# Optimization experiments

Measured on AMD Instinct MI355X. Metric: run time of the kernel, lower is better.

The kernel has to match this reference:

```python
import jax, jax.numpy as jnp
import numpy as np
from jax import lax

ALIVE_THRESHOLD = 0.1
GROWTH_BOOST = 1.0  # forward default arg

_SX = jnp.array([[-1., 0., 1.], [-2., 0., 2.], [-1., 0., 1.]], dtype=jnp.float32)
_SY = jnp.array([[-1., -2., -1.], [0., 0., 0.], [1., 2., 1.]], dtype=jnp.float32)


def _depthwise3x3(x, k):
    # x: [B,C,H,W], k: [3,3] -> depthwise conv, padding 1 (SAME)
    C = x.shape[1]
    w = jnp.tile(k[None, None], (C, 1, 1, 1))  # [C,1,3,3]
    return lax.conv_general_dilated(
        x, w, window_strides=(1, 1), padding='SAME',
        dimension_numbers=('NCHW', 'OIHW', 'NCHW'), feature_group_count=C)


def _avg_pool3x3(x):
    # torch avg_pool2d(k=3, stride=1, pad=1, count_include_pad=True) == sum window / 9 with zero pad
    w = jnp.ones((1, 1, 3, 3), dtype=x.dtype) / 9.0
    return lax.conv_general_dilated(
        x, w, window_strides=(1, 1), padding='SAME',
        dimension_numbers=('NCHW', 'OIHW', 'NCHW'))


def setup_inputs() -> dict:
    key = jax.random.key(0)
    ks = jax.random.split(key, 5)
    B, C, H, W = 16, 8, 512, 512
    x = jax.random.normal(ks[0], (B, C, H, W), dtype=jnp.float32)
    # kaiming_normal_(a=0.3) -> std = sqrt(2/(1+a^2)) / sqrt(fan_in)
    gain = float(np.sqrt(2.0 / (1.0 + 0.3 ** 2)))
    w1 = jax.random.normal(ks[1], (32, 24), dtype=jnp.float32) * (gain / np.sqrt(24))
    w2 = jax.random.normal(ks[2], (32, 32), dtype=jnp.float32) * (gain / np.sqrt(32))
    w3 = jax.random.normal(ks[3], (8, 32), dtype=jnp.float32) * (gain / np.sqrt(32))
    b1 = jnp.full((32,), 0.05, dtype=jnp.float32)
    b2 = jnp.full((32,), 0.05, dtype=jnp.float32)
    b3 = jnp.full((8,), 0.05, dtype=jnp.float32)
    growth_rate = jnp.array([0.3], dtype=jnp.float32)
    return {'x': x, 'w1': w1, 'b1': b1, 'w2': w2, 'b2': b2,
            'w3': w3, 'b3': b3, 'growth_rate': growth_rate}


def reference(x, w1, b1, w2, b2, w3, b3, growth_rate):
    # perceive: [x, sobel_x(x), sobel_y(x)] -> [B, 3C, H, W]
    perceived = jnp.concatenate([x, _depthwise3x3(x, _SX), _depthwise3x3(x, _SY)], axis=1)
    # per-pixel MLP (1x1 convs)
    h = jax.nn.relu(jnp.einsum('bchw,oc->bohw', perceived, w1) + b1[None, :, None, None])
    h = jax.nn.relu(jnp.einsum('bchw,oc->bohw', h, w2) + b2[None, :, None, None])
    dx = jnp.einsum('bchw,oc->bohw', h, w3) + b3[None, :, None, None]
    dx = dx * growth_rate[0] * GROWTH_BOOST
    # alive masking / growth zones
    alive_mask = (x[:, 3:4] > ALIVE_THRESHOLD).astype(x.dtype)
    alive_ratio = jnp.mean(alive_mask)
    neighbor_alive = _avg_pool3x3(alive_mask)
    growth_zones = (neighbor_alive > 0.01).astype(x.dtype) * 0.2  # [B,1,H,W]
    boost = jnp.where(alive_ratio < 0.2, growth_zones, jnp.zeros_like(growth_zones))
    dx = jnp.concatenate([dx[:, :3], dx[:, 3:4] + boost, dx[:, 4:]], axis=1)
    new_x = jnp.clip(x + dx, -1.0, 1.0)
    alpha = jnp.clip(new_x[:, 3:4], 0.0, 1.0)
    return jnp.concatenate([new_x[:, :3], alpha, new_x[:, 4:]], axis=1)
```

## Files before the change

kernel.cpp:

```cpp
#include <hip/hip_runtime.h>

namespace {

constexpr int kH = 512, kW = 512, kB = 16, kC = 8;
constexpr int kHW = kH * kW;
constexpr int kBS = kC * kHW;
constexpr int TW = 64, TH = 4;
constexpr int TWP = TW + 2, THP = TH + 2;

__global__ __launch_bounds__(256)
void alive_count_kernel(const float* __restrict__ x, int* __restrict__ cnt) {
    __shared__ int sdata[4];
    const int tid = threadIdx.x;
    const int total4 = kB * kHW / 4;
    int idx = blockIdx.x * 256 + tid;
    const int stride = gridDim.x * 256;
    int local = 0;
    const float4* x4 = (const float4*)x;
    for (int i = idx; i < total4; i += stride) {
        int b = i >> 16;
        int off = i & 65535;
        float4 v = x4[(size_t)b * (kBS / 4) + (3 * kHW / 4) + off];
        local += (v.x > 0.1f) + (v.y > 0.1f) + (v.z > 0.1f) + (v.w > 0.1f);
    }
    for (int off = 32; off > 0; off >>= 1)
        local += __shfl_down(local, off, 64);
    if ((tid & 63) == 0) sdata[tid >> 6] = local;
    __syncthreads();
    if (tid == 0) atomicAdd(cnt, sdata[0] + sdata[1] + sdata[2] + sdata[3]);
}

__global__ __launch_bounds__(256, 2)
void nca_fused_kernel(const float* __restrict__ x,
                      const float* __restrict__ w1, const float* __restrict__ b1,
                      const float* __restrict__ w2, const float* __restrict__ b2,
                      const float* __restrict__ w3, const float* __restrict__ b3,
                      const float* __restrict__ growth,
                      const int* __restrict__ alive_cnt,
                      float* __restrict__ out) {
    __shared__ float tile[kC][THP][TWP];

    const int w0 = blockIdx.x * TW;
    const int h0 = blockIdx.y * TH;
    const int b  = blockIdx.z;
    const int tid = threadIdx.x;
    const float* xb = x + b * kBS;

    constexpr int TILE_N = kC * THP * TWP;
    for (int i = tid; i < TILE_N; i += 256) {
        int c  = i / (THP * TWP);
        int r  = i - c * (THP * TWP);
        int hh = r / TWP;
        int ww = r - hh * TWP;
        int gh = h0 + hh - 1;
        int gw = w0 + ww - 1;
        float v = 0.0f;
        if ((unsigned)gh < (unsigned)kH && (unsigned)gw < (unsigned)kW)
            v = xb[c * kHW + gh * kW + gw];
        (&tile[0][0][0])[i] = v;
    }
    __syncthreads();

    const int ww = tid & (TW - 1);
    const int hh = tid >> 6;

    float p[24];
    int nalive = 0;
#pragma unroll
    for (int c = 0; c < kC; ++c) {
        float a00 = tile[c][hh    ][ww], a01 = tile[c][hh    ][ww + 1], a02 = tile[c][hh    ][ww + 2];
        float a10 = tile[c][hh + 1][ww], a11 = tile[c][hh + 1][ww + 1], a12 = tile[c][hh + 1][ww + 2];
        float a20 = tile[c][hh + 2][ww], a21 = tile[c][hh + 2][ww + 1], a22 = tile[c][hh + 2][ww + 2];
        p[c]      = a11;
        p[8 + c]  = (a02 - a00) + 2.0f * (a12 - a10) + (a22 - a20);
        p[16 + c] = (a20 - a00) + 2.0f * (a21 - a01) + (a22 - a02);
        if (c == 3) {
            nalive = (a00 > 0.1f) + (a01 > 0.1f) + (a02 > 0.1f)
                   + (a10 > 0.1f) + (a11 > 0.1f) + (a12 > 0.1f)
                   + (a20 > 0.1f) + (a21 > 0.1f) + (a22 > 0.1f);
        }
    }

    float h1[32];
#pragma unroll
    for (int o = 0; o < 32; ++o) {
        float acc = b1[o];
#pragma unroll
        for (int i2 = 0; i2 < 24; ++i2) acc = fmaf(w1[o * 24 + i2], p[i2], acc);
        h1[o] = fmaxf(acc, 0.0f);
    }
    float h2[32];
#pragma unroll
    for (int o = 0; o < 32; ++o) {
        float acc = b2[o];
#pragma unroll
        for (int i2 = 0; i2 < 32; ++i2) acc = fmaf(w2[o * 32 + i2], h1[i2], acc);
        h2[o] = fmaxf(acc, 0.0f);
    }
    float d[8];
#pragma unroll
    for (int o = 0; o < 8; ++o) {
        float acc = b3[o];
#pragma unroll
        for (int i2 = 0; i2 < 32; ++i2) acc = fmaf(w3[o * 32 + i2], h2[i2], acc);
        d[o] = acc;
    }

    const float g = growth[0];
    const float ratio = (float)(*alive_cnt) * (1.0f / 4194304.0f);
    const float boost = (ratio < 0.2f && nalive > 0) ? 0.2f : 0.0f;

    float* ob = out + b * kBS + (h0 + hh) * kW + (w0 + ww);
#pragma unroll
    for (int c = 0; c < kC; ++c) {
        float v = p[c] + d[c] * g + ((c == 3) ? boost : 0.0f);
        const float lo = (c == 3) ? 0.0f : -1.0f;
        v = fminf(fmaxf(v, lo), 1.0f);
        ob[c * kHW] = v;
    }
}

}

extern "C" void kernel_launch(void* const* d_in, const int* in_sizes, int n_in,
                              void* d_out, int out_size, void* d_ws, size_t ws_size,
                              hipStream_t stream) {
    const float* x  = (const float*)d_in[0];
    const float* w1 = (const float*)d_in[1];
    const float* b1 = (const float*)d_in[2];
    const float* w2 = (const float*)d_in[3];
    const float* b2 = (const float*)d_in[4];
    const float* w3 = (const float*)d_in[5];
    const float* b3 = (const float*)d_in[6];
    const float* gr = (const float*)d_in[7];
    float* out = (float*)d_out;
    int* cnt = (int*)d_ws;

    hipMemsetAsync(cnt, 0, sizeof(int), stream);
    alive_count_kernel<<<256, 256, 0, stream>>>(x, cnt);
    dim3 grid(kW / TW, kH / TH, kB);
    nca_fused_kernel<<<grid, 256, 0, stream>>>(x, w1, b1, w2, b2, w3, b3, gr, cnt, out);
}
```

Measured before the change: 479.8 us.

## Run per-pixel MLP on bf16 MFMA with split hi/lo precision emulation

Replaces the scalar FMA loops for the three per-pixel 1x1-conv layers with 16x16x32 bf16 MFMA instructions. Each fp32 operand is split into bf16 hi and lo parts, and four MFMAs per product approximate fp32 accuracy. Layer outputs are rearranged into B fragments with ds_bpermute, and weights are preloaded into register fragments. The alive-count kernel grid is also raised from 256 to 2048 blocks. This aims to cut the dominant VALU FMA cost, at the price of extra conversion, permute and LDS traffic and some loss of precision.

```diff
diff --git a/kernel.cpp b/kernel.cpp
--- a/kernel.cpp
+++ b/kernel.cpp
@@ -1,6 +1,10 @@
 #include <hip/hip_runtime.h>
 
 namespace {
+
+typedef __attribute__((ext_vector_type(8))) short short8;
+typedef __attribute__((ext_vector_type(4))) float f32x4;
+typedef __attribute__((ext_vector_type(4))) unsigned int uint4v;
 
 constexpr int kH = 512, kW = 512, kB = 16, kC = 8;
 constexpr int kHW = kH * kW;
@@ -30,7 +34,66 @@
     if (tid == 0) atomicAdd(cnt, sdata[0] + sdata[1] + sdata[2] + sdata[3]);
 }
 
-__global__ __launch_bounds__(256, 2)
+__device__ inline unsigned int cvt_pk_bf16(float a, float b) {
+    unsigned int r;
+    asm("v_cvt_pk_bf16_f32 %0, %1, %2" : "=v"(r) : "v"(a), "v"(b));
+    return r;
+}
+__device__ inline void split_pair(float a, float b, unsigned int& h, unsigned int& l) {
+    h = cvt_pk_bf16(a, b);
+    float ra = a - __builtin_bit_cast(float, h << 16);
+    float rb = b - __builtin_bit_cast(float, h & 0xffff0000u);
+    l = cvt_pk_bf16(ra, rb);
+}
+__device__ inline short8 frag_of(unsigned int u0, unsigned int u1,
+                                 unsigned int u2, unsigned int u3) {
+    uint4v u = {u0, u1, u2, u3};
+    return __builtin_bit_cast(short8, u);
+}
+__device__ inline void split_frag(f32x4 a, f32x4 b, short8& hi, short8& lo) {
+    unsigned int h0, h1, h2, h3, l0, l1, l2, l3;
+    split_pair(a.x, a.y, h0, l0);
+    split_pair(a.z, a.w, h1, l1);
+    split_pair(b.x, b.y, h2, l2);
+    split_pair(b.z, b.w, h3, l3);
+    hi = frag_of(h0, h1, h2, h3);
+    lo = frag_of(l0, l1, l2, l3);
+}
+__device__ inline f32x4 mfma4(short8 wh, short8 wl, short8 bh, short8 bl, f32x4 acc) {
+    acc = __builtin_amdgcn_mfma_f32_16x16x32_bf16(wh, bh, acc, 0, 0, 0);
+    acc = __builtin_amdgcn_mfma_f32_16x16x32_bf16(wh, bl, acc, 0, 0, 0);
+    acc = __builtin_amdgcn_mfma_f32_16x16x32_bf16(wl, bh, acc, 0, 0, 0);
+    acc = __builtin_amdgcn_mfma_f32_16x16x32_bf16(wl, bl, acc, 0, 0, 0);
+    return acc;
+}
+__device__ inline f32x4 relu4(f32x4 v) {
+    v.x = fmaxf(v.x, 0.f); v.y = fmaxf(v.y, 0.f);
+    v.z = fmaxf(v.z, 0.f); v.w = fmaxf(v.w, 0.f);
+    return v;
+}
+__device__ inline void transpose_to_bfrag(f32x4 v0, f32x4 v1, int i1, int i2,
+                                          bool oddq, bool lowq,
+                                          short8& bh, short8& bl) {
+    unsigned int Ah, Al, Bh, Bl, Ch, Cl, Dh, Dl;
+    split_pair(v0.x, v0.y, Ah, Al);
+    split_pair(v0.z, v0.w, Bh, Bl);
+    split_pair(v1.x, v1.y, Ch, Cl);
+    split_pair(v1.z, v1.w, Dh, Dl);
+    int f1h = __builtin_amdgcn_ds_bpermute(i1, (int)(oddq ? Ch : Ah));
+    int f2h = __builtin_amdgcn_ds_bpermute(i2, (int)(oddq ? Ah : Ch));
+    int f3h = __builtin_amdgcn_ds_bpermute(i1, (int)(oddq ? Dh : Bh));
+    int f4h = __builtin_amdgcn_ds_bpermute(i2, (int)(oddq ? Bh : Dh));
+    int f1l = __builtin_amdgcn_ds_bpermute(i1, (int)(oddq ? Cl : Al));
+    int f2l = __builtin_amdgcn_ds_bpermute(i2, (int)(oddq ? Al : Cl));
+    int f3l = __builtin_amdgcn_ds_bpermute(i1, (int)(oddq ? Dl : Bl));
+    int f4l = __builtin_amdgcn_ds_bpermute(i2, (int)(oddq ? Bl : Dl));
+    bh = frag_of(lowq ? (unsigned)f1h : (unsigned)f2h, lowq ? (unsigned)f3h : (unsigned)f4h,
+                 lowq ? (unsigned)f2h : (unsigned)f1h, lowq ? (unsigned)f4h : (unsigned)f3h);
+    bl = frag_of(lowq ? (unsigned)f1l : (unsigned)f2l, lowq ? (unsigned)f3l : (unsigned)f4l,
+                 lowq ? (unsigned)f2l : (unsigned)f1l, lowq ? (unsigned)f4l : (unsigned)f3l);
+}
+
+__global__ __launch_bounds__(256)
 void nca_fused_kernel(const float* __restrict__ x,
                       const float* __restrict__ w1, const float* __restrict__ b1,
                       const float* __restrict__ w2, const float* __restrict__ b2,
@@ -39,21 +102,60 @@
                       const int* __restrict__ alive_cnt,
                       float* __restrict__ out) {
     __shared__ float tile[kC][THP][TWP];
+    __shared__ __align__(16) unsigned int s_hi[4][64][20];
+    __shared__ __align__(16) unsigned int s_lo[4][64][20];
+    __shared__ __align__(16) float s_d[4][64][8];
 
     const int w0 = blockIdx.x * TW;
     const int h0 = blockIdx.y * TH;
     const int b  = blockIdx.z;
     const int tid = threadIdx.x;
+    const int lane = tid & 63;
+    const int wv = tid >> 6;
+    const int m = lane & 15;
+    const int q = lane >> 4;
+    const bool oddq = (q & 1) != 0;
+    const bool lowq = q < 2;
+    const int brq = ((q & 1) << 1) | (q >> 1);
+    const int i1 = (m + 16 * brq) << 2;
+    const int i2 = (m + 16 * (brq ^ 1)) << 2;
     const float* xb = x + b * kBS;
+
+    f32x4 zero4 = {0.f, 0.f, 0.f, 0.f};
+    short8 w1h[2], w1l[2], w2h[2], w2l[2], w3h, w3l;
+    f32x4 bias1[2], bias2[2], bias3;
+#pragma unroll
+    for (int mo = 0; mo < 2; ++mo) {
+        int o = mo * 16 + m;
+        int off = (q < 3) ? (o * 24 + q * 8) : 0;
+        f32x4 wa = *(const f32x4*)(w1 + off);
+        f32x4 wb = *(const f32x4*)(w1 + off + 4);
+        if (q == 3) { wa = zero4; wb = zero4; }
+        split_frag(wa, wb, w1h[mo], w1l[mo]);
+        f32x4 wc = *(const f32x4*)(w2 + o * 32 + q * 8);
+        f32x4 wd = *(const f32x4*)(w2 + o * 32 + q * 8 + 4);
+        split_frag(wc, wd, w2h[mo], w2l[mo]);
+        bias1[mo] = *(const f32x4*)(b1 + mo * 16 + q * 4);
+        bias2[mo] = *(const f32x4*)(b2 + mo * 16 + q * 4);
+    }
+    {
+        int off3 = (m < 8) ? (m * 32 + q * 8) : 0;
+        f32x4 wa = *(const f32x4*)(w3 + off3);
+        f32x4 wb = *(const f32x4*)(w3 + off3 + 4);
+        if (m >= 8) { wa = zero4; wb = zero4; }
+        split_frag(wa, wb, w3h, w3l);
+        bias3 = zero4;
+        if (lowq) bias3 = *(const f32x4*)(b3 + q * 4);
+    }
 
     constexpr int TILE_N = kC * THP * TWP;
     for (int i = tid; i < TILE_N; i += 256) {
         int c  = i / (THP * TWP);
-        int r  = i - c * (THP * TWP);
-        int hh = r / TWP;
-        int ww = r - hh * TWP;
-        int gh = h0 + hh - 1;
-        int gw = w0 + ww - 1;
+        int rr = i - c * (THP * TWP);
+        int th = rr / TWP;
+        int tw = rr - th * TWP;
+        int gh = h0 + th - 1;
+        int gw = w0 + tw - 1;
         float v = 0.0f;
         if ((unsigned)gh < (unsigned)kH && (unsigned)gw < (unsigned)kW)
             v = xb[c * kHW + gh * kW + gw];
@@ -61,14 +163,13 @@
     }
     __syncthreads();
 
-    const int ww = tid & (TW - 1);
-    const int hh = tid >> 6;
-
+    const int ww = lane;
+    const int hh = wv;
     float p[24];
     int nalive = 0;
 #pragma unroll
     for (int c = 0; c < kC; ++c) {
-        float a00 = tile[c][hh    ][ww], a01 = tile[c][hh    ][ww + 1], a02 = tile[c][hh    ][ww + 2];
+        float a00 = tile[c][hh][ww],     a01 = tile[c][hh][ww + 1],     a02 = tile[c][hh][ww + 2];
         float a10 = tile[c][hh + 1][ww], a11 = tile[c][hh + 1][ww + 1], a12 = tile[c][hh + 1][ww + 2];
         float a20 = tile[c][hh + 2][ww], a21 = tile[c][hh + 2][ww + 1], a22 = tile[c][hh + 2][ww + 2];
         p[c]      = a11;
@@ -80,40 +181,58 @@
                    + (a20 > 0.1f) + (a21 > 0.1f) + (a22 > 0.1f);
         }
     }
-
-    float h1[32];
-#pragma unroll
-    for (int o = 0; o < 32; ++o) {
-        float acc = b1[o];
-#pragma unroll
-        for (int i2 = 0; i2 < 24; ++i2) acc = fmaf(w1[o * 24 + i2], p[i2], acc);
-        h1[o] = fmaxf(acc, 0.0f);
-    }
-    float h2[32];
-#pragma unroll
-    for (int o = 0; o < 32; ++o) {
-        float acc = b2[o];
-#pragma unroll
-        for (int i2 = 0; i2 < 32; ++i2) acc = fmaf(w2[o * 32 + i2], h1[i2], acc);
-        h2[o] = fmaxf(acc, 0.0f);
-    }
-    float d[8];
-#pragma unroll
-    for (int o = 0; o < 8; ++o) {
-        float acc = b3[o];
-#pragma unroll
-        for (int i2 = 0; i2 < 32; ++i2) acc = fmaf(w3[o * 32 + i2], h2[i2], acc);
-        d[o] = acc;
-    }
-
+#pragma unroll
+    for (int gg = 0; gg < 3; ++gg) {
+        unsigned int ha, hb, hc, hd, la, lb, lc, ld;
+        split_pair(p[8 * gg + 0], p[8 * gg + 1], ha, la);
+        split_pair(p[8 * gg + 2], p[8 * gg + 3], hb, lb);
+        split_pair(p[8 * gg + 4], p[8 * gg + 5], hc, lc);
+        split_pair(p[8 * gg + 6], p[8 * gg + 7], hd, ld);
+        uint4v uh = {ha, hb, hc, hd};
+        uint4v ul = {la, lb, lc, ld};
+        *(uint4v*)&s_hi[wv][lane][gg * 4] = uh;
+        *(uint4v*)&s_lo[wv][lane][gg * 4] = ul;
+    }
+    {
+        uint4v z = {0u, 0u, 0u, 0u};
+        *(uint4v*)&s_hi[wv][lane][12] = z;
+        *(uint4v*)&s_lo[wv][lane][12] = z;
+    }
+
+#pragma unroll
+    for (int np = 0; np < 4; ++np) {
+        const int r = np * 16 + m;
+        short8 bh = __builtin_bit_cast(short8, *(const uint4v*)&s_hi[wv][r][q * 4]);
+        short8 bl = __builtin_bit_cast(short8, *(const uint4v*)&s_lo[wv][r][q * 4]);
+        f32x4 acc0 = bias1[0], acc1 = bias1[1];
+        acc0 = mfma4(w1h[0], w1l[0], bh, bl, acc0);
+        acc1 = mfma4(w1h[1], w1l[1], bh, bl, acc1);
+        acc0 = relu4(acc0); acc1 = relu4(acc1);
+        short8 b2fh, b2fl;
+        transpose_to_bfrag(acc0, acc1, i1, i2, oddq, lowq, b2fh, b2fl);
+        f32x4 acc2a = bias2[0], acc2b = bias2[1];
+        acc2a = mfma4(w2h[0], w2l[0], b2fh, b2fl, acc2a);
+        acc2b = mfma4(w2h[1], w2l[1], b2fh, b2fl, acc2b);
+        acc2a = relu4(acc2a); acc2b = relu4(acc2b);
+        short8 b3fh, b3fl;
+        transpose_to_bfrag(acc2a, acc2b, i1, i2, oddq, lowq, b3fh, b3fl);
+        f32x4 acc3 = bias3;
+        acc3 = mfma4(w3h, w3l, b3fh, b3fl, acc3);
+        if (lowq) {
+            *(f32x4*)&s_d[wv][r][q * 4] = acc3;
+        }
+    }
+
+    f32x4 dA = *(const f32x4*)&s_d[wv][lane][0];
+    f32x4 dB = *(const f32x4*)&s_d[wv][lane][4];
+    float dv[8] = {dA.x, dA.y, dA.z, dA.w, dB.x, dB.y, dB.z, dB.w};
     const float g = growth[0];
     const float ratio = (float)(*alive_cnt) * (1.0f / 4194304.0f);
     const float boost = (ratio < 0.2f && nalive > 0) ? 0.2f : 0.0f;
-
     float* ob = out + b * kBS + (h0 + hh) * kW + (w0 + ww);
 #pragma unroll
     for (int c = 0; c < kC; ++c) {
-        float v = p[c] + d[c] * g + ((c == 3) ? boost : 0.0f);
+        float v = p[c] + dv[c] * g + ((c == 3) ? boost : 0.0f);
         const float lo = (c == 3) ? 0.0f : -1.0f;
         v = fminf(fmaxf(v, lo), 1.0f);
         ob[c * kHW] = v;
@@ -137,7 +256,7 @@
     int* cnt = (int*)d_ws;
 
     hipMemsetAsync(cnt, 0, sizeof(int), stream);
-    alive_count_kernel<<<256, 256, 0, stream>>>(x, cnt);
+    alive_count_kernel<<<2048, 256, 0, stream>>>(x, cnt);
     dim3 grid(kW / TW, kH / TH, kB);
     nca_fused_kernel<<<grid, 256, 0, stream>>>(x, w1, b1, w2, b2, w3, b3, gr, cnt, out);
 }
```

Result: slower. 565.9 us (+18.0%).
